# Optimization experiments

Hardware: AMD Instinct MI355X
Metric: run time of the kernel (lower is better)

The kernel has to match this reference:

```python
import jax, jax.numpy as jnp
import numpy as np

N = 100000        # nodes
E = 3200000       # edges (before self-loops)
F_IN = 16         # data.num_features
H = 2             # heads (both layers)
C1, C2 = 8, 4     # per-head out channels of conv1 / conv2
NEG_SLOPE = 0.2   # PyG GATConv default


def setup_inputs() -> dict:
    key = jax.random.key(0)
    ks = jax.random.split(key, 10)
    x = jax.random.normal(ks[0], (N, F_IN), jnp.float32)
    edge_index = jax.random.randint(ks[1], (2, E), 0, N)  # [src; dst]

    def glorot(k, shape):
        fan = shape[0] + shape[-1]
        return jax.random.normal(k, shape, jnp.float32) * jnp.sqrt(2.0 / fan)

    # conv1: 16 -> 8, heads=2 (concat -> 16)
    W1 = glorot(ks[2], (F_IN, H * C1))
    att_src1 = glorot(ks[3], (H, C1))
    att_dst1 = glorot(ks[4], (H, C1))
    b1 = jnp.zeros((H * C1,), jnp.float32)
    # conv2: 16 -> 4, heads=2 (concat -> 8)
    W2 = glorot(ks[5], (H * C1, H * C2))
    att_src2 = glorot(ks[6], (H, C2))
    att_dst2 = glorot(ks[7], (H, C2))
    b2 = jnp.zeros((H * C2,), jnp.float32)
    return {"x": x, "edge_index": edge_index,
            "W1": W1, "att_src1": att_src1, "att_dst1": att_dst1, "b1": b1,
            "W2": W2, "att_src2": att_src2, "att_dst2": att_dst2, "b2": b2}


def gat_conv(x, src, dst, W, a_src, a_dst, b):
    """PyG-style GATConv: gather + edge logits + per-dst segment softmax + scatter."""
    n = x.shape[0]
    h_heads, c = a_src.shape
    h = (x @ W).reshape(n, h_heads, c)                       # [N,H,C]
    al_s = jnp.einsum('nhc,hc->nh', h, a_src)                # [N,H]
    al_d = jnp.einsum('nhc,hc->nh', h, a_dst)                # [N,H]
    e = jax.nn.leaky_relu(al_s[src] + al_d[dst], NEG_SLOPE)  # [E,H]
    m = jax.ops.segment_max(e, dst, num_segments=n)          # per-dst max
    m = jnp.where(jnp.isfinite(m), m, 0.0)
    w = jnp.exp(e - m[dst])
    z = jax.ops.segment_sum(w, dst, num_segments=n)
    alpha = w / (z[dst] + 1e-16)                             # [E,H]
    out = jax.ops.segment_sum(alpha[:, :, None] * h[src], dst, num_segments=n)
    return out.reshape(n, h_heads * c) + b


def reference(x, edge_index, W1, att_src1, att_dst1, b1, W2, att_src2, att_dst2, b2):
    n = x.shape[0]
    loop = jnp.arange(n, dtype=edge_index.dtype)             # add_self_loops=True
    src = jnp.concatenate([edge_index[0], loop])
    dst = jnp.concatenate([edge_index[1], loop])
    h = gat_conv(x, src, dst, W1, att_src1, att_dst1, b1)
    h = jax.nn.elu(h)
    # dropout(p=0.6, training=self.training) -> identity in eval mode
    return gat_conv(h, src, dst, W2, att_src2, att_dst2, b2)
```

## Files before the change

### kernel.cpp

```cpp
#include <hip/hip_runtime.h>
#include <hip/hip_bf16.h>

#define TB 128
#define TBB 1024
#define BSH 8
#define BSZ 256
#define CHUNK 8192
#define EBP 512
#define TLS 1024

__device__ __forceinline__ float ldany(const void* __restrict__ p, size_t i, int isf32) {
  if (isf32) return ((const float*)p)[i];
  unsigned int u = ((const unsigned short*)p)[i];
  return __uint_as_float(u << 16);
}

__device__ __forceinline__ unsigned f2bf2(float lo, float hi) {
  unsigned ul = __float_as_uint(lo), uh = __float_as_uint(hi);
  ul += 0x7FFFu + ((ul >> 16) & 1u);
  uh += 0x7FFFu + ((uh >> 16) & 1u);
  return (ul >> 16) | (uh & 0xFFFF0000u);
}
__device__ __forceinline__ unsigned short f2bf1(float x) {
  unsigned u = __float_as_uint(x);
  u += 0x7FFFu + ((u >> 16) & 1u);
  return (unsigned short)(u >> 16);
}
__device__ __forceinline__ float bf_lo(unsigned u) { return __uint_as_float(u << 16); }
__device__ __forceinline__ float bf_hi(unsigned u) { return __uint_as_float(u & 0xFFFF0000u); }

__device__ __forceinline__ int detect_isf(const unsigned short* __restrict__ xb) {
  int lane = threadIdx.x & 63;
  int mx = 0;
  #pragma unroll
  for (int j = 0; j < 4; ++j) { int e = (xb[lane * 4 + j] >> 7) & 0xFF; mx = max(mx, e); }
  #pragma unroll
  for (int off = 32; off > 0; off >>= 1) mx = max(mx, __shfl_xor(mx, off));
  return mx > 160;
}

__global__ __launch_bounds__(TBB) void
k_bcount_proj(const int* __restrict__ ei, int E, int Et, int NB, int EB,
              int* __restrict__ bcnt,
              const unsigned short* __restrict__ xb,
              const void* __restrict__ Wg, const void* __restrict__ adg,
              unsigned* __restrict__ hb, float* __restrict__ ald, int n) {
  __shared__ int shmem[512];
  if (blockIdx.x < EB) {
    int* lcnt = shmem;
    for (int i = threadIdx.x; i < NB; i += TBB) lcnt[i] = 0;
    __syncthreads();
    long b0 = (long)blockIdx.x * CHUNK;
    int cnt = (int)(((long)Et - b0 < (long)CHUNK) ? ((long)Et - b0) : (long)CHUNK);
    for (int i = threadIdx.x * 4; i < cnt; i += TBB * 4) {
      long e = b0 + i;
      int rem = cnt - i;
      if (rem >= 4 && e + 3 < (long)E) {
        int4 d4 = *(const int4*)(ei + E + e);
        atomicAdd(&lcnt[d4.x >> BSH], 1);
        atomicAdd(&lcnt[d4.y >> BSH], 1);
        atomicAdd(&lcnt[d4.z >> BSH], 1);
        atomicAdd(&lcnt[d4.w >> BSH], 1);
      } else {
        int m = rem < 4 ? rem : 4;
        for (int j = 0; j < m; ++j) {
          long ee = e + j;
          int d = (ee < E) ? ei[E + ee] : (int)(ee - E);
          atomicAdd(&lcnt[d >> BSH], 1);
        }
      }
    }
    __syncthreads();
    for (int i = threadIdx.x; i < NB; i += TBB)
      bcnt[(size_t)i * EBP + blockIdx.x] = lcnt[i];
  } else {
    const int isf = detect_isf(xb);
    float* Ws = (float*)shmem;
    __shared__ float ad_s[16];
    for (int i = threadIdx.x; i < 256; i += TBB) Ws[i] = ldany(Wg, i, isf);
    if (threadIdx.x < 16) ad_s[threadIdx.x] = ldany(adg, threadIdx.x, isf);
    __syncthreads();
    int nid = (blockIdx.x - EB) * TBB + threadIdx.x;
    if (nid >= n) return;

    float xr[16];
    #pragma unroll
    for (int i = 0; i < 16; ++i) xr[i] = ldany(xb, (size_t)nid * 16 + i, isf);

    float hv[16];
    #pragma unroll
    for (int j = 0; j < 16; ++j) hv[j] = 0.f;
    #pragma unroll
    for (int k = 0; k < 16; ++k) {
      #pragma unroll
      for (int j = 0; j < 16; ++j) hv[j] += xr[k] * Ws[k * 16 + j];
    }

    unsigned* row = hb + (size_t)nid * 8;
    ((uint4*)row)[0] = make_uint4(f2bf2(hv[0], hv[1]),  f2bf2(hv[2], hv[3]),
                                  f2bf2(hv[4], hv[5]),  f2bf2(hv[6], hv[7]));
    ((uint4*)row)[1] = make_uint4(f2bf2(hv[8], hv[9]),  f2bf2(hv[10], hv[11]),
                                  f2bf2(hv[12], hv[13]), f2bf2(hv[14], hv[15]));

    float d0 = 0.f, d1 = 0.f;
    #pragma unroll
    for (int c = 0; c < 8; ++c) {
      d0 += hv[c] * ad_s[c];
      d1 += hv[8 + c] * ad_s[8 + c];
    }
    ((float2*)ald)[nid] = make_float2(d0, d1);
  }
}

__global__ __launch_bounds__(EBP) void k_blockpfx(int* __restrict__ bcnt,
                                                  int* __restrict__ gcnt,
                                                  int EB, int NB) {
  __shared__ int sh[EBP];
  const int bk = blockIdx.x;
  const int tid = threadIdx.x;
  int v = (tid < EB) ? bcnt[(size_t)bk * EBP + tid] : 0;
  sh[tid] = v;
  __syncthreads();
  for (int off = 1; off < EBP; off <<= 1) {
    int t = (tid >= off) ? sh[tid - off] : 0;
    __syncthreads();
    sh[tid] += t;
    __syncthreads();
  }
  if (tid < EB) bcnt[(size_t)bk * EBP + tid] = sh[tid] - v;
  if (tid == 0) gcnt[bk] = sh[EBP - 1];
}

__global__ void k_bscan(const int* __restrict__ gcnt, int* __restrict__ gbase,
                        int NB, int Et) {
  __shared__ int sh[1024];
  int tid = threadIdx.x;
  int v = (tid < NB) ? gcnt[tid] : 0;
  sh[tid] = v;
  __syncthreads();
  for (int off = 1; off < 1024; off <<= 1) {
    int t = (tid >= off) ? sh[tid - off] : 0;
    __syncthreads();
    sh[tid] += t;
    __syncthreads();
  }
  if (tid < NB) gbase[tid] = sh[tid] - v;
  if (tid == 0) gbase[NB] = Et;
}

__global__ __launch_bounds__(TBB) void k_bscatter(const int* __restrict__ ei, int E, int Et,
                                                  int NB, const int* __restrict__ gbase,
                                                  const int* __restrict__ bcnt,
                                                  int* __restrict__ packed) {
  __shared__ int lcur[512];
  const int b = blockIdx.x;
  for (int i = threadIdx.x; i < NB; i += TBB)
    lcur[i] = gbase[i] + bcnt[(size_t)i * EBP + b];
  __syncthreads();
  long b0 = (long)b * CHUNK;
  int cnt = (int)(((long)Et - b0 < (long)CHUNK) ? ((long)Et - b0) : (long)CHUNK);
  for (int i = threadIdx.x * 4; i < cnt; i += TBB * 4) {
    long e = b0 + i;
    int rem = cnt - i;
    if (rem >= 4 && e + 3 < (long)E) {
      int4 s4 = *(const int4*)(ei + e);
      int4 d4 = *(const int4*)(ei + E + e);
      int bk, pos;
      bk = d4.x >> BSH; pos = atomicAdd(&lcur[bk], 1); packed[pos] = ((d4.x & (BSZ-1)) << 17) | s4.x;
      bk = d4.y >> BSH; pos = atomicAdd(&lcur[bk], 1); packed[pos] = ((d4.y & (BSZ-1)) << 17) | s4.y;
      bk = d4.z >> BSH; pos = atomicAdd(&lcur[bk], 1); packed[pos] = ((d4.z & (BSZ-1)) << 17) | s4.z;
      bk = d4.w >> BSH; pos = atomicAdd(&lcur[bk], 1); packed[pos] = ((d4.w & (BSZ-1)) << 17) | s4.w;
    } else {
      int m = rem < 4 ? rem : 4;
      for (int j = 0; j < m; ++j) {
        long ee = e + j;
        int s, d;
        if (ee < E) { s = ei[ee]; d = ei[E + ee]; }
        else        { s = (int)(ee - E); d = s; }
        int bk = d >> BSH;
        int pos = atomicAdd(&lcur[bk], 1);
        packed[pos] = ((d & (BSZ - 1)) << 17) | s;
      }
    }
  }
}

__global__ __launch_bounds__(TLS) void k_localsort(const int* __restrict__ gbase,
                                                   const int* __restrict__ packed,
                                                   int* __restrict__ rowptr,
                                                   int* __restrict__ csr,
                                                   int n, int Et) {
  __shared__ int lcnt[BSZ], lbase[BSZ], sh[BSZ];
  const int b = blockIdx.x;
  const int node0 = b << BSH;
  const int tid = threadIdx.x;
  if (tid < BSZ) lcnt[tid] = 0;
  __syncthreads();
  const int beg = gbase[b], end = gbase[b + 1];
  for (int k = beg + tid; k < end; k += TLS)
    atomicAdd(&lcnt[packed[k] >> 17], 1);
  __syncthreads();
  int v = (tid < BSZ) ? lcnt[tid] : 0;
  if (tid < BSZ) sh[tid] = v;
  __syncthreads();
  for (int off = 1; off < BSZ; off <<= 1) {
    int t = (tid < BSZ && tid >= off) ? sh[tid - off] : 0;
    __syncthreads();
    if (tid < BSZ) sh[tid] += t;
    __syncthreads();
  }
  if (tid < BSZ) lbase[tid] = sh[tid] - v;
  __syncthreads();
  const int nn = min(BSZ, n - node0);
  if (tid < nn) rowptr[node0 + tid] = beg + lbase[tid];
  if (b == 0 && tid == 0) rowptr[n] = Et;
  for (int k = beg + tid; k < end; k += TLS) {
    int p = packed[k];
    int dl = p >> 17;
    int pos = beg + atomicAdd(&lbase[dl], 1);
    csr[pos] = p & 0x1FFFF;
  }
}

__global__ __launch_bounds__(TB) void
gat_gather1(const int* __restrict__ rowptr, const int* __restrict__ csr,
            const unsigned* __restrict__ hb, const float* __restrict__ ald,
            const void* __restrict__ bias, const void* __restrict__ as1g,
            const void* __restrict__ W2g, const void* __restrict__ ad2g,
            unsigned* __restrict__ hb2, float* __restrict__ ald2,
            int n, const unsigned short* __restrict__ xb) {
  const int isf = detect_isf(xb);
  __shared__ float sb[16];
  __shared__ float as1s[16];
  __shared__ float sv[8 * 17];
  __shared__ float sh2[8 * 9];
  __shared__ float W2s[128];
  __shared__ float ad2s[8];
  if (threadIdx.x < 16) sb[threadIdx.x] = ldany(bias, threadIdx.x, isf);
  if (threadIdx.x >= 16 && threadIdx.x < 32) as1s[threadIdx.x - 16] = ldany(as1g, threadIdx.x - 16, isf);
  if (threadIdx.x >= 32 && threadIdx.x < 40) ad2s[threadIdx.x - 32] = ldany(ad2g, threadIdx.x - 32, isf);
  if (threadIdx.x < 128) W2s[threadIdx.x] = ldany(W2g, threadIdx.x, isf);
  __syncthreads();

  const int t = blockIdx.x * TB + threadIdx.x;
  const int sub = t & 15, nid = t >> 4;
  const int slot = sub >> 1, hq = sub & 1;
  const bool act = nid < n;
  int beg = 0, end = 0;
  float aldv = 0.f;
  float as_r[8];
  #pragma unroll
  for (int c = 0; c < 8; ++c) as_r[c] = as1s[hq * 8 + c];
  if (act) {
    beg = rowptr[nid];
    end = rowptr[nid + 1];
    aldv = ald[(size_t)nid * 2 + hq];
  }

  float acc[8];
  #pragma unroll
  for (int c = 0; c < 8; ++c) acc[c] = 0.f;
  float z = 0.f;

  int k  = beg + slot;
  int kn = k + 8;
  int s_cur = (k  < end) ? csr[k]  : 0;
  int s_nxt = (kn < end) ? csr[kn] : 0;
  uint4 u_cur = *(const uint4*)(hb + (size_t)s_cur * 8 + hq * 4);
  while (k < end) {
    uint4 u_n = *(const uint4*)(hb + (size_t)s_nxt * 8 + hq * 4);
    int kf = kn + 8;
    int s_f = (kf < end) ? csr[kf] : 0;
    float h0 = bf_lo(u_cur.x), h1 = bf_hi(u_cur.x);
    float h2 = bf_lo(u_cur.y), h3 = bf_hi(u_cur.y);
    float h4 = bf_lo(u_cur.z), h5 = bf_hi(u_cur.z);
    float h6 = bf_lo(u_cur.w), h7 = bf_hi(u_cur.w);
    float alsv = h0 * as_r[0] + h1 * as_r[1] + h2 * as_r[2] + h3 * as_r[3]
               + h4 * as_r[4] + h5 * as_r[5] + h6 * as_r[6] + h7 * as_r[7];
    float lg = alsv + aldv;
    lg = lg > 0.f ? lg : 0.2f * lg;
    float w = __expf(lg);
    z += w;
    acc[0] += w * h0; acc[1] += w * h1; acc[2] += w * h2; acc[3] += w * h3;
    acc[4] += w * h4; acc[5] += w * h5; acc[6] += w * h6; acc[7] += w * h7;
    k = kn; kn = kf; s_cur = s_nxt; s_nxt = s_f; u_cur = u_n;
  }

  #pragma unroll
  for (int off = 2; off < 16; off <<= 1) {
    z += __shfl_xor(z, off);
    #pragma unroll
    for (int c = 0; c < 8; ++c) acc[c] += __shfl_xor(acc[c], off);
  }
  float inv = 1.f / (z + 1e-16f);

  if (act && slot == 0) {
    int ns = threadIdx.x >> 4;
    #pragma unroll
    for (int c = 0; c < 8; ++c) {
      float v = acc[c] * inv + sb[hq * 8 + c];
      v = v > 0.f ? v : expm1f(v);
      sv[ns * 17 + hq * 8 + c] = v;
    }
  }
  __syncthreads();
  {
    int j = threadIdx.x;
    if (j < 64) {
      int ns = j >> 3, out = j & 7;
      int nid2 = blockIdx.x * 8 + ns;
      if (nid2 < n) {
        float h2v = 0.f;
        #pragma unroll
        for (int kk = 0; kk < 16; ++kk) h2v += sv[ns * 17 + kk] * W2s[kk * 8 + out];
        ((unsigned short*)hb2)[(size_t)nid2 * 8 + out] = f2bf1(h2v);
        sh2[ns * 9 + out] = h2v;
      }
    }
  }
  __syncthreads();
  {
    int j = threadIdx.x;
    if (j < 8) {
      int nid2 = blockIdx.x * 8 + j;
      if (nid2 < n) {
        float d20 = 0.f, d21 = 0.f;
        #pragma unroll
        for (int c = 0; c < 4; ++c) {
          d20 += sh2[j * 9 + c] * ad2s[c];
          d21 += sh2[j * 9 + 4 + c] * ad2s[4 + c];
        }
        ((float2*)ald2)[nid2] = make_float2(d20, d21);
      }
    }
  }
}

__global__ __launch_bounds__(TB) void
gat_gather2(const int* __restrict__ rowptr, const int* __restrict__ csr,
            const unsigned* __restrict__ hb2, const float* __restrict__ ald2,
            const void* __restrict__ bias, const void* __restrict__ as2g,
            void* __restrict__ outp, int n, const unsigned short* __restrict__ xb) {
  const int isf = detect_isf(xb);
  __shared__ float sb[8];
  __shared__ float as2s[8];
  if (threadIdx.x < 8) sb[threadIdx.x] = ldany(bias, threadIdx.x, isf);
  if (threadIdx.x >= 8 && threadIdx.x < 16) as2s[threadIdx.x - 8] = ldany(as2g, threadIdx.x - 8, isf);
  __syncthreads();

  const int t = blockIdx.x * TB + threadIdx.x;
  const int sub = t & 15, nid = t >> 4;
  const int slot = sub >> 1, hq = sub & 1;
  const bool act = nid < n;
  int beg = 0, end = 0;
  float aldv = 0.f;
  float as_r[4];
  #pragma unroll
  for (int c = 0; c < 4; ++c) as_r[c] = as2s[hq * 4 + c];
  if (act) {
    beg = rowptr[nid];
    end = rowptr[nid + 1];
    aldv = ald2[(size_t)nid * 2 + hq];
  }

  float a0 = 0.f, a1 = 0.f, a2 = 0.f, a3 = 0.f, z = 0.f;

  int k  = beg + slot;
  int kn = k + 8;
  int s_cur = (k  < end) ? csr[k]  : 0;
  int s_nxt = (kn < end) ? csr[kn] : 0;
  uint2 u_cur = *(const uint2*)(hb2 + (size_t)s_cur * 4 + hq * 2);
  while (k < end) {
    uint2 u_n = *(const uint2*)(hb2 + (size_t)s_nxt * 4 + hq * 2);
    int kf = kn + 8;
    int s_f = (kf < end) ? csr[kf] : 0;
    float h0 = bf_lo(u_cur.x), h1 = bf_hi(u_cur.x);
    float h2 = bf_lo(u_cur.y), h3 = bf_hi(u_cur.y);
    float alsv = h0 * as_r[0] + h1 * as_r[1] + h2 * as_r[2] + h3 * as_r[3];
    float lg = alsv + aldv;
    lg = lg > 0.f ? lg : 0.2f * lg;
    float w = __expf(lg);
    z += w;
    a0 += w * h0; a1 += w * h1; a2 += w * h2; a3 += w * h3;
    k = kn; kn = kf; s_cur = s_nxt; s_nxt = s_f; u_cur = u_n;
  }

  #pragma unroll
  for (int off = 2; off < 16; off <<= 1) {
    z  += __shfl_xor(z, off);
    a0 += __shfl_xor(a0, off); a1 += __shfl_xor(a1, off);
    a2 += __shfl_xor(a2, off); a3 += __shfl_xor(a3, off);
  }

  if (act && slot == 0) {
    float inv = 1.f / (z + 1e-16f);
    float v0 = a0 * inv + sb[hq * 4 + 0];
    float v1 = a1 * inv + sb[hq * 4 + 1];
    float v2 = a2 * inv + sb[hq * 4 + 2];
    float v3 = a3 * inv + sb[hq * 4 + 3];
    if (isf) {
      ((float4*)outp)[(size_t)nid * 2 + hq] = make_float4(v0, v1, v2, v3);
    } else {
      ((uint2*)outp)[(size_t)nid * 2 + hq] = make_uint2(f2bf2(v0, v1), f2bf2(v2, v3));
    }
  }
}

extern "C" void kernel_launch(void* const* d_in, const int* in_sizes, int n_in,
                              void* d_out, int out_size, void* d_ws, size_t ws_size,
                              hipStream_t stream) {
  const unsigned short* xb = (const unsigned short*)d_in[0];
  const int*  ei  = (const int*)d_in[1];
  const void* W1  = d_in[2];
  const void* as1 = d_in[3];
  const void* ad1 = d_in[4];
  const void* b1  = d_in[5];
  const void* W2  = d_in[6];
  const void* as2 = d_in[7];
  const void* ad2 = d_in[8];
  const void* b2  = d_in[9];

  const int n  = in_sizes[0] / 16;
  const int E  = in_sizes[1] / 2;
  const int Et = E + n;
  const int NB = (n + BSZ - 1) >> BSH;
  const int EB = (Et + CHUNK - 1) / CHUNK;

  char* base = (char*)d_ws;
  int* gcnt   = (int*)(base + 64);
  int* gbase_ = gcnt + (NB + 1);
  int* rowptr = gbase_ + (NB + 1);
  int* bcnt   = rowptr + (n + 1);
  int* csr    = bcnt + (size_t)NB * EBP;
  int* packed = csr + Et;
  size_t off1 = 64 + sizeof(int) * ((size_t)(NB + 1) * 2 + (size_t)(n + 1)
                                    + (size_t)NB * EBP + 2 * (size_t)Et);
  off1 = (off1 + 255) & ~(size_t)255;
  unsigned* hb1  = (unsigned*)(base + off1);
  float*    ald1 = (float*)(base + off1 + (size_t)32 * n);
  size_t off2 = off1 + (size_t)40 * n;
  off2 = (off2 + 255) & ~(size_t)255;
  unsigned* hb2  = (unsigned*)(base + off2);
  float*    ald2 = (float*)(base + off2 + (size_t)16 * n);

  const int pblk = (n + TBB - 1) / TBB;
  const int gblk = (16 * n + TB - 1) / TB;

  k_bcount_proj<<<EB + pblk, TBB, 0, stream>>>(ei, E, Et, NB, EB, bcnt,
                                               xb, W1, ad1, hb1, ald1, n);
  k_blockpfx<<<NB, EBP, 0, stream>>>(bcnt, gcnt, EB, NB);
  k_bscan<<<1, 1024, 0, stream>>>(gcnt, gbase_, NB, Et);
  k_bscatter<<<EB, TBB, 0, stream>>>(ei, E, Et, NB, gbase_, bcnt, packed);
  k_localsort<<<NB, TLS, 0, stream>>>(gbase_, packed, rowptr, csr, n, Et);

  gat_gather1<<<gblk, TB, 0, stream>>>(rowptr, csr, hb1, ald1, b1, as1,
                                       W2, ad2, hb2, ald2, n, xb);

  gat_gather2<<<gblk, TB, 0, stream>>>(rowptr, csr, hb2, ald2, b2, as2,
                                       d_out, n, xb);
}
```

Before: 123.5 us.

## Fold bucket scan into scatter/localsort, shuffle-based layer-2 projection, wider gather2 loads

Removes the single-block k_bscan launch: each k_bscatter block now redoes the bucket-count prefix scan itself, and k_localsort computes its segment base by summing the preceding bucket counts. In gat_gather1, the shared-memory staging and block barriers for the W2 projection and the att_dst2 dot product are replaced by warp shuffles, and the block size grows to 256. gat_gather2 now has each lane process both heads with 128-bit loads and a stride of 16 over edges, instead of one head per lane with a stride of 8. This trades a kernel launch and some barriers for redundant scan work in every block and more registers per lane.

```diff
diff --git a/kernel.cpp b/kernel.cpp
--- a/kernel.cpp
+++ b/kernel.cpp
@@ -1,7 +1,7 @@
 #include <hip/hip_runtime.h>
 #include <hip/hip_bf16.h>
 
-#define TB 128
+#define TB 256
 #define TBB 1024
 #define BSH 8
 #define BSZ 256
@@ -131,35 +131,28 @@
   if (tid == 0) gcnt[bk] = sh[EBP - 1];
 }
 
-__global__ void k_bscan(const int* __restrict__ gcnt, int* __restrict__ gbase,
-                        int NB, int Et) {
-  __shared__ int sh[1024];
-  int tid = threadIdx.x;
-  int v = (tid < NB) ? gcnt[tid] : 0;
-  sh[tid] = v;
-  __syncthreads();
-  for (int off = 1; off < 1024; off <<= 1) {
-    int t = (tid >= off) ? sh[tid - off] : 0;
-    __syncthreads();
-    sh[tid] += t;
-    __syncthreads();
-  }
-  if (tid < NB) gbase[tid] = sh[tid] - v;
-  if (tid == 0) gbase[NB] = Et;
-}
-
 __global__ __launch_bounds__(TBB) void k_bscatter(const int* __restrict__ ei, int E, int Et,
-                                                  int NB, const int* __restrict__ gbase,
+                                                  int NB, const int* __restrict__ gcnt,
                                                   const int* __restrict__ bcnt,
                                                   int* __restrict__ packed) {
+  __shared__ int sh[512];
   __shared__ int lcur[512];
   const int b = blockIdx.x;
-  for (int i = threadIdx.x; i < NB; i += TBB)
-    lcur[i] = gbase[i] + bcnt[(size_t)i * EBP + b];
+  const int tid = threadIdx.x;
+  int v = 0;
+  if (tid < 512) { v = (tid < NB) ? gcnt[tid] : 0; sh[tid] = v; }
+  __syncthreads();
+  for (int off = 1; off < 512; off <<= 1) {
+    int t = (tid < 512 && tid >= off) ? sh[tid - off] : 0;
+    __syncthreads();
+    if (tid < 512) sh[tid] += t;
+    __syncthreads();
+  }
+  if (tid < NB) lcur[tid] = (sh[tid] - v) + bcnt[(size_t)tid * EBP + b];
   __syncthreads();
   long b0 = (long)b * CHUNK;
   int cnt = (int)(((long)Et - b0 < (long)CHUNK) ? ((long)Et - b0) : (long)CHUNK);
-  for (int i = threadIdx.x * 4; i < cnt; i += TBB * 4) {
+  for (int i = tid * 4; i < cnt; i += TBB * 4) {
     long e = b0 + i;
     int rem = cnt - i;
     if (rem >= 4 && e + 3 < (long)E) {
@@ -185,18 +178,33 @@
   }
 }
 
-__global__ __launch_bounds__(TLS) void k_localsort(const int* __restrict__ gbase,
+__global__ __launch_bounds__(TLS) void k_localsort(const int* __restrict__ gcnt,
                                                    const int* __restrict__ packed,
                                                    int* __restrict__ rowptr,
                                                    int* __restrict__ csr,
-                                                   int n, int Et) {
+                                                   int n, int Et, int NB) {
   __shared__ int lcnt[BSZ], lbase[BSZ], sh[BSZ];
+  __shared__ int red[16];
+  __shared__ int s_beg, s_end;
   const int b = blockIdx.x;
   const int node0 = b << BSH;
   const int tid = threadIdx.x;
+  int partial = 0;
+  for (int i = tid; i < b; i += TLS) partial += gcnt[i];
+  #pragma unroll
+  for (int off = 32; off > 0; off >>= 1) partial += __shfl_xor(partial, off);
+  if ((tid & 63) == 0) red[tid >> 6] = partial;
   if (tid < BSZ) lcnt[tid] = 0;
   __syncthreads();
-  const int beg = gbase[b], end = gbase[b + 1];
+  if (tid == 0) {
+    int s = 0;
+    #pragma unroll
+    for (int i = 0; i < 16; ++i) s += red[i];
+    s_beg = s;
+    s_end = s + gcnt[b];
+  }
+  __syncthreads();
+  const int beg = s_beg, end = s_end;
   for (int k = beg + tid; k < end; k += TLS)
     atomicAdd(&lcnt[packed[k] >> 17], 1);
   __syncthreads();
@@ -232,14 +240,12 @@
   const int isf = detect_isf(xb);
   __shared__ float sb[16];
   __shared__ float as1s[16];
-  __shared__ float sv[8 * 17];
-  __shared__ float sh2[8 * 9];
   __shared__ float W2s[128];
   __shared__ float ad2s[8];
   if (threadIdx.x < 16) sb[threadIdx.x] = ldany(bias, threadIdx.x, isf);
   if (threadIdx.x >= 16 && threadIdx.x < 32) as1s[threadIdx.x - 16] = ldany(as1g, threadIdx.x - 16, isf);
   if (threadIdx.x >= 32 && threadIdx.x < 40) ad2s[threadIdx.x - 32] = ldany(ad2g, threadIdx.x - 32, isf);
-  if (threadIdx.x < 128) W2s[threadIdx.x] = ldany(W2g, threadIdx.x, isf);
+  if (threadIdx.x >= 128) W2s[threadIdx.x - 128] = ldany(W2g, threadIdx.x - 128, isf);
   __syncthreads();
 
   const int t = blockIdx.x * TB + threadIdx.x;
@@ -294,46 +300,30 @@
   }
   float inv = 1.f / (z + 1e-16f);
 
-  if (act && slot == 0) {
-    int ns = threadIdx.x >> 4;
-    #pragma unroll
-    for (int c = 0; c < 8; ++c) {
-      float v = acc[c] * inv + sb[hq * 8 + c];
-      v = v > 0.f ? v : expm1f(v);
-      sv[ns * 17 + hq * 8 + c] = v;
-    }
-  }
-  __syncthreads();
-  {
-    int j = threadIdx.x;
-    if (j < 64) {
-      int ns = j >> 3, out = j & 7;
-      int nid2 = blockIdx.x * 8 + ns;
-      if (nid2 < n) {
-        float h2v = 0.f;
-        #pragma unroll
-        for (int kk = 0; kk < 16; ++kk) h2v += sv[ns * 17 + kk] * W2s[kk * 8 + out];
-        ((unsigned short*)hb2)[(size_t)nid2 * 8 + out] = f2bf1(h2v);
-        sh2[ns * 9 + out] = h2v;
-      }
-    }
-  }
-  __syncthreads();
-  {
-    int j = threadIdx.x;
-    if (j < 8) {
-      int nid2 = blockIdx.x * 8 + j;
-      if (nid2 < n) {
-        float d20 = 0.f, d21 = 0.f;
-        #pragma unroll
-        for (int c = 0; c < 4; ++c) {
-          d20 += sh2[j * 9 + c] * ad2s[c];
-          d21 += sh2[j * 9 + 4 + c] * ad2s[4 + c];
-        }
-        ((float2*)ald2)[nid2] = make_float2(d20, d21);
-      }
-    }
-  }
+  float v_[8];
+  #pragma unroll
+  for (int c = 0; c < 8; ++c) {
+    float v = acc[c] * inv + sb[hq * 8 + c];
+    v_[c] = v > 0.f ? v : expm1f(v);
+  }
+
+  const int lg = (threadIdx.x & 63) & ~15;
+  const int out = sub & 7;
+  float h2v = 0.f;
+  #pragma unroll
+  for (int kk = 0; kk < 16; ++kk) {
+    float vk = __shfl(v_[kk & 7], lg + (kk >> 3));
+    h2v += vk * W2s[kk * 8 + out];
+  }
+  if (act && sub < 8)
+    ((unsigned short*)hb2)[(size_t)nid * 8 + out] = f2bf1(h2v);
+
+  float part = h2v * ad2s[out];
+  part += __shfl_xor(part, 1);
+  part += __shfl_xor(part, 2);
+  float d21 = __shfl(part, lg + 4);
+  if (act && sub == 0)
+    ((float2*)ald2)[nid] = make_float2(part, d21);
 }
 
 __global__ __launch_bounds__(TB) void
@@ -350,58 +340,67 @@
 
   const int t = blockIdx.x * TB + threadIdx.x;
   const int sub = t & 15, nid = t >> 4;
-  const int slot = sub >> 1, hq = sub & 1;
   const bool act = nid < n;
   int beg = 0, end = 0;
-  float aldv = 0.f;
-  float as_r[4];
-  #pragma unroll
-  for (int c = 0; c < 4; ++c) as_r[c] = as2s[hq * 4 + c];
+  float ald0 = 0.f, ald1 = 0.f;
+  float as_r[8];
+  #pragma unroll
+  for (int c = 0; c < 8; ++c) as_r[c] = as2s[c];
   if (act) {
     beg = rowptr[nid];
     end = rowptr[nid + 1];
-    aldv = ald2[(size_t)nid * 2 + hq];
-  }
-
-  float a0 = 0.f, a1 = 0.f, a2 = 0.f, a3 = 0.f, z = 0.f;
-
-  int k  = beg + slot;
-  int kn = k + 8;
+    float2 ad = ((const float2*)ald2)[nid];
+    ald0 = ad.x; ald1 = ad.y;
+  }
+
+  float a[8];
+  #pragma unroll
+  for (int c = 0; c < 8; ++c) a[c] = 0.f;
+  float z0 = 0.f, z1 = 0.f;
+
+  int k  = beg + sub;
+  int kn = k + 16;
   int s_cur = (k  < end) ? csr[k]  : 0;
   int s_nxt = (kn < end) ? csr[kn] : 0;
-  uint2 u_cur = *(const uint2*)(hb2 + (size_t)s_cur * 4 + hq * 2);
+  uint4 u_cur = *(const uint4*)(hb2 + (size_t)s_cur * 4);
   while (k < end) {
-    uint2 u_n = *(const uint2*)(hb2 + (size_t)s_nxt * 4 + hq * 2);
-    int kf = kn + 8;
+    uint4 u_n = *(const uint4*)(hb2 + (size_t)s_nxt * 4);
+    int kf = kn + 16;
     int s_f = (kf < end) ? csr[kf] : 0;
     float h0 = bf_lo(u_cur.x), h1 = bf_hi(u_cur.x);
     float h2 = bf_lo(u_cur.y), h3 = bf_hi(u_cur.y);
-    float alsv = h0 * as_r[0] + h1 * as_r[1] + h2 * as_r[2] + h3 * as_r[3];
-    float lg = alsv + aldv;
-    lg = lg > 0.f ? lg : 0.2f * lg;
-    float w = __expf(lg);
-    z += w;
-    a0 += w * h0; a1 += w * h1; a2 += w * h2; a3 += w * h3;
+    float h4 = bf_lo(u_cur.z), h5 = bf_hi(u_cur.z);
+    float h6 = bf_lo(u_cur.w), h7 = bf_hi(u_cur.w);
+    float ls0 = h0 * as_r[0] + h1 * as_r[1] + h2 * as_r[2] + h3 * as_r[3];
+    float ls1 = h4 * as_r[4] + h5 * as_r[5] + h6 * as_r[6] + h7 * as_r[7];
+    float lg0 = ls0 + ald0, lg1 = ls1 + ald1;
+    lg0 = lg0 > 0.f ? lg0 : 0.2f * lg0;
+    lg1 = lg1 > 0.f ? lg1 : 0.2f * lg1;
+    float w0 = __expf(lg0), w1 = __expf(lg1);
+    z0 += w0; z1 += w1;
+    a[0] += w0 * h0; a[1] += w0 * h1; a[2] += w0 * h2; a[3] += w0 * h3;
+    a[4] += w1 * h4; a[5] += w1 * h5; a[6] += w1 * h6; a[7] += w1 * h7;
     k = kn; kn = kf; s_cur = s_nxt; s_nxt = s_f; u_cur = u_n;
   }
 
   #pragma unroll
-  for (int off = 2; off < 16; off <<= 1) {
-    z  += __shfl_xor(z, off);
-    a0 += __shfl_xor(a0, off); a1 += __shfl_xor(a1, off);
-    a2 += __shfl_xor(a2, off); a3 += __shfl_xor(a3, off);
-  }
-
-  if (act && slot == 0) {
-    float inv = 1.f / (z + 1e-16f);
-    float v0 = a0 * inv + sb[hq * 4 + 0];
-    float v1 = a1 * inv + sb[hq * 4 + 1];
-    float v2 = a2 * inv + sb[hq * 4 + 2];
-    float v3 = a3 * inv + sb[hq * 4 + 3];
+  for (int off = 1; off < 16; off <<= 1) {
+    z0 += __shfl_xor(z0, off); z1 += __shfl_xor(z1, off);
+    #pragma unroll
+    for (int c = 0; c < 8; ++c) a[c] += __shfl_xor(a[c], off);
+  }
+
+  if (act && sub == 0) {
+    float inv0 = 1.f / (z0 + 1e-16f), inv1 = 1.f / (z1 + 1e-16f);
+    float v[8];
+    #pragma unroll
+    for (int c = 0; c < 8; ++c) v[c] = a[c] * (c < 4 ? inv0 : inv1) + sb[c];
     if (isf) {
-      ((float4*)outp)[(size_t)nid * 2 + hq] = make_float4(v0, v1, v2, v3);
+      ((float4*)outp)[(size_t)nid * 2 + 0] = make_float4(v[0], v[1], v[2], v[3]);
+      ((float4*)outp)[(size_t)nid * 2 + 1] = make_float4(v[4], v[5], v[6], v[7]);
     } else {
-      ((uint2*)outp)[(size_t)nid * 2 + hq] = make_uint2(f2bf2(v0, v1), f2bf2(v2, v3));
+      ((uint4*)outp)[nid] = make_uint4(f2bf2(v[0], v[1]), f2bf2(v[2], v[3]),
+                                       f2bf2(v[4], v[5]), f2bf2(v[6], v[7]));
     }
   }
 }
@@ -428,12 +427,11 @@
 
   char* base = (char*)d_ws;
   int* gcnt   = (int*)(base + 64);
-  int* gbase_ = gcnt + (NB + 1);
-  int* rowptr = gbase_ + (NB + 1);
+  int* rowptr = gcnt + (NB + 1);
   int* bcnt   = rowptr + (n + 1);
   int* csr    = bcnt + (size_t)NB * EBP;
   int* packed = csr + Et;
-  size_t off1 = 64 + sizeof(int) * ((size_t)(NB + 1) * 2 + (size_t)(n + 1)
+  size_t off1 = 64 + sizeof(int) * ((size_t)(NB + 1) + (size_t)(n + 1)
                                     + (size_t)NB * EBP + 2 * (size_t)Et);
   off1 = (off1 + 255) & ~(size_t)255;
   unsigned* hb1  = (unsigned*)(base + off1);
@@ -449,9 +447,8 @@
   k_bcount_proj<<<EB + pblk, TBB, 0, stream>>>(ei, E, Et, NB, EB, bcnt,
                                                xb, W1, ad1, hb1, ald1, n);
   k_blockpfx<<<NB, EBP, 0, stream>>>(bcnt, gcnt, EB, NB);
-  k_bscan<<<1, 1024, 0, stream>>>(gcnt, gbase_, NB, Et);
-  k_bscatter<<<EB, TBB, 0, stream>>>(ei, E, Et, NB, gbase_, bcnt, packed);
-  k_localsort<<<NB, TLS, 0, stream>>>(gbase_, packed, rowptr, csr, n, Et);
+  k_bscatter<<<EB, TBB, 0, stream>>>(ei, E, Et, NB, gcnt, bcnt, packed);
+  k_localsort<<<NB, TLS, 0, stream>>>(gcnt, packed, rowptr, csr, n, Et, NB);
 
   gat_gather1<<<gblk, TB, 0, stream>>>(rowptr, csr, hb1, ald1, b1, as1,
                                        W2, ad2, hb2, ald2, n, xb);
```

New measurement: 127.0 us. +2.9%, slower.
